# Kernel tuning notes

Hardware: AMD Instinct MI355X
Metric: run time of the kernel (lower is better)

The kernel has to match this reference:

```python
import jax, jax.numpy as jnp
import numpy as np

EPS = 1e-5

def layer_norm(x, gamma):
    mu = jnp.mean(x, axis=-1, keepdims=True)
    var = jnp.mean(jnp.square(x - mu), axis=-1, keepdims=True)
    return (x - mu) / jnp.sqrt(var + EPS) * gamma

def setup_inputs() -> dict:
    key = jax.random.key(0)
    ks = jax.random.split(key, 10)
    b, n, j = 2, 2048, 2048
    dim, ctx_dim, heads, dim_head, ff_mult = 1024, 1024, 16, 64, 4
    inner = heads * dim_head
    ff_inner = ff_mult * dim
    s = 0.02
    return {
        'x': jax.random.normal(ks[0], (b, n, dim), jnp.float32),
        'context': jax.random.normal(ks[1], (b, j, ctx_dim), jnp.float32),
        'mask': jax.random.randint(ks[2], (b, j), 0, 2, jnp.int32),
        'gamma': jnp.ones((dim,), jnp.float32),
        'ctx_gamma': jnp.ones((ctx_dim,), jnp.float32),
        'Wq': jax.random.normal(ks[3], (dim, inner), jnp.float32) * s,
        'Wkv': jax.random.normal(ks[4], (ctx_dim, 2 * dim_head), jnp.float32) * s,
        'Wout': jax.random.normal(ks[5], (inner, dim), jnp.float32) * s,
        'Wff1': jax.random.normal(ks[6], (dim, 2 * ff_inner), jnp.float32) * s,
        'Wff2': jax.random.normal(ks[7], (ff_inner, dim), jnp.float32) * s,
    }

def reference(x, context, mask, gamma, ctx_gamma, Wq, Wkv, Wout, Wff1, Wff2):
    heads, dim_head = 16, 64
    b, n, dim = x.shape
    scale = dim_head ** -0.5
    xn = layer_norm(x, gamma)                              # [b,n,dim]
    ctx = layer_norm(context, ctx_gamma)                   # [b,j,cd]
    q = (xn @ Wq).reshape(b, n, heads, dim_head).transpose(0, 2, 1, 3) * scale  # [b,h,n,d]
    kv = ctx @ Wkv                                         # [b,j,2d]
    k, v = kv[..., :dim_head], kv[..., dim_head:]          # [b,j,d] each (multi-query)
    sim = jnp.einsum('bhid,bjd->bhij', q, k)               # [b,h,n,j]
    sim = jnp.where((mask == 0)[:, None, None, :], -jnp.inf, sim)
    attn = jax.nn.softmax(sim, axis=-1)
    out = jnp.einsum('bhij,bjd->bhid', attn, v)            # [b,h,n,d]
    out = out.transpose(0, 2, 1, 3).reshape(b, n, heads * dim_head)
    out = out @ Wout                                       # [b,n,dim]
    # parallel SwiGLU FF on normalized x
    h = xn @ Wff1
    ff_inner = Wff2.shape[0]
    a, gate = h[..., :ff_inner], h[..., ff_inner:]
    out = out + (jax.nn.silu(gate) * a) @ Wff2
    return out
```

## Files before the change

kernel.cpp:

```cpp
#include <hip/hip_runtime.h>

typedef unsigned short u16;
typedef unsigned int   u32;
typedef __bf16  bf16x8 __attribute__((ext_vector_type(8)));
typedef __bf16  bf16x2 __attribute__((ext_vector_type(2)));
typedef float   f32x4  __attribute__((ext_vector_type(4)));

static __device__ __forceinline__ float b2f(u16 v) {
    return __builtin_bit_cast(float, (u32)(((u32)v) << 16));
}
static __device__ __forceinline__ u16 f2b(float f) {
    u32 u = __builtin_bit_cast(u32, f);
    return (u16)((u + 0x7FFFu + ((u >> 16) & 1u)) >> 16);
}
static __device__ __forceinline__ u32 pack2(float a, float b) {
    bf16x2 t; t[0] = (__bf16)a; t[1] = (__bf16)b;
    return __builtin_bit_cast(u32, t);
}

__global__ __launch_bounds__(256)
void ln_kernel(const float* __restrict__ x, const float* __restrict__ ctx,
               const float* __restrict__ gamma, const float* __restrict__ cgamma,
               u16* __restrict__ xn, u16* __restrict__ ctxn)
{
    const int row = blockIdx.x;
    const int tid = threadIdx.x;
    const float* src; const float* g; u16* dst;
    if (row < 4096) { src = x   + (long)row * 1024;          g = gamma;  dst = xn   + (long)row * 1024; }
    else            { src = ctx + (long)(row - 4096) * 1024; g = cgamma; dst = ctxn + (long)(row - 4096) * 1024; }
    float4 v = ((const float4*)src)[tid];
    float s = v.x + v.y + v.z + v.w;
    float q = v.x*v.x + v.y*v.y + v.z*v.z + v.w*v.w;
#pragma unroll
    for (int off = 32; off; off >>= 1) { s += __shfl_xor(s, off); q += __shfl_xor(q, off); }
    __shared__ float r1[4], r2[4];
    if ((tid & 63) == 0) { r1[tid >> 6] = s; r2[tid >> 6] = q; }
    __syncthreads();
    s = r1[0] + r1[1] + r1[2] + r1[3];
    q = r2[0] + r2[1] + r2[2] + r2[3];
    float mu   = s * (1.0f / 1024.0f);
    float var  = q * (1.0f / 1024.0f) - mu * mu;
    float rstd = rsqrtf(var + 1e-5f);
    float4 gv = ((const float4*)g)[tid];
    ushort4 o;
    o.x = f2b((v.x - mu) * rstd * gv.x);
    o.y = f2b((v.y - mu) * rstd * gv.y);
    o.z = f2b((v.z - mu) * rstd * gv.z);
    o.w = f2b((v.w - mu) * rstd * gv.w);
    ((ushort4*)dst)[tid] = o;
}

__global__ __launch_bounds__(256)
void wconv(const float* __restrict__ W, u16* __restrict__ Wt, int N, int K, float scale)
{
    __shared__ float tile[32][33];
    const int tid = threadIdx.x;
    const int n0 = blockIdx.x * 32;
    const int k0 = blockIdx.y * 32;
    const int r  = tid >> 3;
    const int c4 = (tid & 7) * 4;
    float4 v = *(const float4*)&W[(long)(k0 + r) * N + n0 + c4];
    tile[r][c4 + 0] = v.x; tile[r][c4 + 1] = v.y; tile[r][c4 + 2] = v.z; tile[r][c4 + 3] = v.w;
    __syncthreads();
    ushort4 o;
    o.x = f2b(tile[c4 + 0][r] * scale);
    o.y = f2b(tile[c4 + 1][r] * scale);
    o.z = f2b(tile[c4 + 2][r] * scale);
    o.w = f2b(tile[c4 + 3][r] * scale);
    *(ushort4*)&Wt[(long)(n0 + r) * K + k0 + c4] = o;
}

__global__ __launch_bounds__(256)
void wconv_ff1(const float* __restrict__ W, u16* __restrict__ Wt)
{
    __shared__ float tile[32][33];
    const int tid = threadIdx.x;
    const int a  = blockIdx.x;
    const int k0 = blockIdx.y * 32;
    const int r  = tid >> 3;
    const int c4 = (tid & 7) * 4;
    const int srccol = (c4 < 16) ? (a * 16 + c4) : (4096 + a * 16 + (c4 - 16));
    float4 v = *(const float4*)&W[(long)(k0 + r) * 8192 + srccol];
    tile[r][c4 + 0] = v.x; tile[r][c4 + 1] = v.y; tile[r][c4 + 2] = v.z; tile[r][c4 + 3] = v.w;
    __syncthreads();
    ushort4 o;
    o.x = f2b(tile[c4 + 0][r]);
    o.y = f2b(tile[c4 + 1][r]);
    o.z = f2b(tile[c4 + 2][r]);
    o.w = f2b(tile[c4 + 3][r]);
    *(ushort4*)&Wt[(long)(a * 32 + r) * 1024 + k0 + c4] = o;
}

__global__ __launch_bounds__(256)
void kext_build(const float* __restrict__ kvf, const int* __restrict__ mask,
                u16* __restrict__ kext, float* __restrict__ mbias)
{
    const int gid = blockIdx.x * 256 + threadIdx.x;
    const int b = gid >> 14;
    const int rem = gid & 16383;
    const int j = rem >> 3;
    const int c = rem & 7;
    const float* src = &kvf[((long)b * 2048 + j) * 128 + c * 8];
    u16 ov[8];
#pragma unroll
    for (int e = 0; e < 8; ++e) ov[e] = f2b(src[e]);
    uint4 w;
    w.x = (u32)ov[0] | ((u32)ov[1] << 16);
    w.y = (u32)ov[2] | ((u32)ov[3] << 16);
    w.z = (u32)ov[4] | ((u32)ov[5] << 16);
    w.w = (u32)ov[6] | ((u32)ov[7] << 16);
    *(uint4*)&kext[((long)b * 2048 + j) * 64 + c * 8] = w;
    if (c == 0) mbias[b * 2048 + j] = mask[b * 2048 + j] ? 0.0f : -1e30f;
}

__global__ __launch_bounds__(256)
void vtrans(const float* __restrict__ kvf, u16* __restrict__ vT)
{
    const int j = blockIdx.x * 256 + threadIdx.x;
    const int d = blockIdx.y;
    const int b = blockIdx.z;
    vT[(long)b * 64 * 2048 + (long)d * 2048 + j] =
        f2b(kvf[((long)b * 2048 + j) * 128 + 64 + d]);
}

#define BM 128
#define BN 128
#define BK 32

template<int EPI>
__global__ __launch_bounds__(256, 2)
void gemm_bt(const u16* __restrict__ A, const u16* __restrict__ Bt,
             void* __restrict__ Cv,
             int K, int lda, int ldb, int ldc,
             long aH, long bH, long cH)
{
    __shared__ __align__(16) u16 sm[2][2][BM * BK];
    const int tid  = threadIdx.x;
    const int wave = tid >> 6;
    const int lane = tid & 63;
    const int tn = blockIdx.x * BN;
    const int tm = blockIdx.y * BM;
    const int z  = blockIdx.z;
    A  += (long)z * aH;
    Bt += (long)z * bH;

    const int arow0 = (tid >> 2);
    const int arow1 = 64 + (tid >> 2);
    const int acs0  = (tid & 3) ^ ((arow0 >> 1) & 3);
    const int acs1  = (tid & 3) ^ ((arow1 >> 1) & 3);
    const int nt = K / BK;

#define STAGE(buf, k0)                                                                              \
    do {                                                                                            \
        __builtin_amdgcn_global_load_lds(                                                           \
            (const __attribute__((address_space(1))) void*)(A + (long)(tm + arow0) * lda + (k0) + acs0 * 8),   \
            (__attribute__((address_space(3))) void*)(&sm[buf][0][(wave * 64) * 8]), 16, 0, 0);     \
        __builtin_amdgcn_global_load_lds(                                                           \
            (const __attribute__((address_space(1))) void*)(A + (long)(tm + arow1) * lda + (k0) + acs1 * 8),   \
            (__attribute__((address_space(3))) void*)(&sm[buf][0][(256 + wave * 64) * 8]), 16, 0, 0); \
        __builtin_amdgcn_global_load_lds(                                                           \
            (const __attribute__((address_space(1))) void*)(Bt + (long)(tn + arow0) * ldb + (k0) + acs0 * 8),  \
            (__attribute__((address_space(3))) void*)(&sm[buf][1][(wave * 64) * 8]), 16, 0, 0);     \
        __builtin_amdgcn_global_load_lds(                                                           \
            (const __attribute__((address_space(1))) void*)(Bt + (long)(tn + arow1) * ldb + (k0) + acs1 * 8),  \
            (__attribute__((address_space(3))) void*)(&sm[buf][1][(256 + wave * 64) * 8]), 16, 0, 0); \
    } while (0)

    STAGE(0, 0);

    f32x4 acc[4][4] = {};
    const int wr   = (wave >> 1) * 64;
    const int wc   = (wave & 1) * 64;
    const int frow = lane & 15;
    const int fk   = lane >> 4;

    for (int t = 0; t < nt; ++t) {
        __syncthreads();
        if (t + 1 < nt) STAGE((t + 1) & 1, (t + 1) * BK);
        const int cur = t & 1;
        bf16x8 af[4], bf[4];
#pragma unroll
        for (int m = 0; m < 4; ++m) {
            int row = wr + m * 16 + frow;
            af[m] = *(const bf16x8*)&sm[cur][0][row * BK + ((fk ^ ((row >> 1) & 3)) * 8)];
        }
#pragma unroll
        for (int n = 0; n < 4; ++n) {
            int row = wc + n * 16 + frow;
            bf[n] = *(const bf16x8*)&sm[cur][1][row * BK + ((fk ^ ((row >> 1) & 3)) * 8)];
        }
#pragma unroll
        for (int m = 0; m < 4; ++m)
#pragma unroll
            for (int n = 0; n < 4; ++n)
                acc[m][n] = __builtin_amdgcn_mfma_f32_16x16x32_bf16(af[m], bf[n], acc[m][n], 0, 0, 0);
    }
#undef STAGE

    const long coff = (long)z * cH;
#pragma unroll
    for (int m = 0; m < 4; ++m) {
        const int row0 = tm + wr + m * 16 + fk * 4;
#pragma unroll
        for (int n = 0; n < 4; ++n) {
            const int col = tn + wc + n * 16 + frow;
#pragma unroll
            for (int r = 0; r < 4; ++r) {
                const long off = coff + (long)(row0 + r) * ldc + col;
                const float v = acc[m][n][r];
                if constexpr (EPI == 0)      ((u16*)Cv)[off] = f2b(v);
                else if constexpr (EPI == 1) ((float*)Cv)[off] = v;
                else if constexpr (EPI == 2) ((float*)Cv)[off] += v;
                else                         atomicAdd(&((float*)Cv)[off], v);
            }
        }
    }
}

template<int EPI>
__global__ __launch_bounds__(512, 2)
void gemm256(const u16* __restrict__ A, const u16* __restrict__ Bt,
             void* __restrict__ Cv, int K, int lda, int ldb, int ldc,
             long aH, long bH)
{
    __shared__ __align__(16) u16 As[2][256 * 64];
    __shared__ __align__(16) u16 Bs[2][256 * 64];
    const int tid  = threadIdx.x;
    const int wave = tid >> 6, lane = tid & 63;
    const int wm = wave >> 2, wn = wave & 3;
    const int frow = lane & 15, fk = lane >> 4;
    const int tn = blockIdx.x * 256;
    const int tm = blockIdx.y * 256;
    const int z  = blockIdx.z;
    A  += (long)z * aH;
    Bt += (long)z * bH;
    const int nt = K >> 6;

    const int lrow  = lane >> 3;
    const int csrc8 = ((lane & 7) ^ lrow) * 8;
    int rbA0[2], rbA1[2], rbB0[2], rbB1[2];
#pragma unroll
    for (int g = 0; g < 2; ++g) {
        const int c = g * 8 + wave;
        const int a0 = ((c >> 3) * 128) + ((c & 7) * 8);
        rbA0[g] = a0; rbA1[g] = a0 + 64;
        const int b0 = ((c >> 2) * 64) + ((c & 3) * 8);
        rbB0[g] = b0; rbB1[g] = b0 + 32;
    }

#define STG(LDS, buf, src, toff, ld, kt, rb)                                                        \
    __builtin_amdgcn_global_load_lds(                                                               \
        (const __attribute__((address_space(1))) void*)((src) + (long)((toff) + (rb) + lrow) * (ld) + ((kt) << 6) + csrc8), \
        (__attribute__((address_space(3))) void*)(&LDS[buf][(rb) * 64]), 16, 0, 0)

#define STAGE_A0(buf, kt) do { STG(As, buf, A,  tm, lda, kt, rbA0[0]); STG(As, buf, A,  tm, lda, kt, rbA0[1]); } while (0)
#define STAGE_A1(buf, kt) do { STG(As, buf, A,  tm, lda, kt, rbA1[0]); STG(As, buf, A,  tm, lda, kt, rbA1[1]); } while (0)
#define STAGE_B0(buf, kt) do { STG(Bs, buf, Bt, tn, ldb, kt, rbB0[0]); STG(Bs, buf, Bt, tn, ldb, kt, rbB0[1]); } while (0)
#define STAGE_B1(buf, kt) do { STG(Bs, buf, Bt, tn, ldb, kt, rbB1[0]); STG(Bs, buf, Bt, tn, ldb, kt, rbB1[1]); } while (0)

#define DSREAD_A(dst, half)                                                                         \
    do { _Pragma("unroll") for (int i = 0; i < 4; ++i) {                                            \
        const int row = wm * 128 + (half) * 64 + i * 16 + frow;                                     \
        _Pragma("unroll") for (int kk = 0; kk < 2; ++kk)                                            \
            dst[i][kk] = *(const bf16x8*)&As[cur][row * 64 + (((kk * 4 + fk) ^ (row & 7)) * 8)];    \
    } } while (0)
#define DSREAD_B(dst, half)                                                                         \
    do { _Pragma("unroll") for (int j = 0; j < 2; ++j) {                                            \
        const int row = wn * 64 + (half) * 32 + j * 16 + frow;                                      \
        _Pragma("unroll") for (int kk = 0; kk < 2; ++kk)                                            \
            dst[j][kk] = *(const bf16x8*)&Bs[cur][row * 64 + (((kk * 4 + fk) ^ (row & 7)) * 8)];    \
    } } while (0)
#define MFMA_Q(afr, bfr, mh, nh)                                                                    \
    do { __builtin_amdgcn_s_setprio(1);                                                             \
    _Pragma("unroll") for (int kk = 0; kk < 2; ++kk)                                                \
        _Pragma("unroll") for (int i = 0; i < 4; ++i)                                               \
            _Pragma("unroll") for (int j = 0; j < 2; ++j)                                           \
                acc[(mh) * 4 + i][(nh) * 2 + j] = __builtin_amdgcn_mfma_f32_16x16x32_bf16(          \
                    afr[i][kk], bfr[j][kk], acc[(mh) * 4 + i][(nh) * 2 + j], 0, 0, 0);              \
    __builtin_amdgcn_s_setprio(0); } while (0)
#define LGKM0 do { asm volatile("s_waitcnt lgkmcnt(0)" ::: "memory"); __builtin_amdgcn_sched_barrier(0); } while (0)
#define SB    __builtin_amdgcn_sched_barrier(0)
#define BAR   __builtin_amdgcn_s_barrier()

    STAGE_B0(0, 0); STAGE_A0(0, 0); STAGE_A1(0, 0); STAGE_B1(0, 0);
    if (nt > 1) {
        STAGE_B0(1, 1); STAGE_A0(1, 1);
        asm volatile("s_waitcnt vmcnt(4)" ::: "memory");
    } else {
        asm volatile("s_waitcnt vmcnt(0)" ::: "memory");
    }
    SB;
    BAR;

    f32x4 acc[8][4] = {};
    bf16x8 a0f[4][2], a1f[4][2], b0f[2][2], b1f[2][2];

    for (int t = 0; t < nt; ++t) {
        const int cur = t & 1, nxt = cur ^ 1;
        DSREAD_A(a0f, 0); DSREAD_B(b0f, 0);
        if (t + 1 < nt) STAGE_A1(nxt, t + 1);
        BAR; LGKM0;
        MFMA_Q(a0f, b0f, 0, 0);
        SB; BAR;
        DSREAD_B(b1f, 1);
        if (t + 1 < nt) STAGE_B1(nxt, t + 1);
        BAR; LGKM0;
        MFMA_Q(a0f, b1f, 0, 1);
        SB; BAR;
        DSREAD_A(a1f, 1);
        if (t + 2 < nt) STAGE_B0(cur, t + 2);
        BAR; LGKM0;
        MFMA_Q(a1f, b1f, 1, 1);
        SB; BAR;
        if (t + 2 < nt) STAGE_A0(cur, t + 2);
        BAR;
        MFMA_Q(a1f, b0f, 1, 0);
        SB;
        if (t + 1 < nt) {
            if (t + 2 < nt) asm volatile("s_waitcnt vmcnt(4)" ::: "memory");
            else            asm volatile("s_waitcnt vmcnt(0)" ::: "memory");
            SB;
            BAR;
        }
    }
#undef BAR
#undef SB
#undef LGKM0
#undef MFMA_Q
#undef DSREAD_A
#undef DSREAD_B
#undef STAGE_A0
#undef STAGE_A1
#undef STAGE_B0
#undef STAGE_B1
#undef STG

    if constexpr (EPI == 3) {
        u16* C = (u16*)Cv;
#pragma unroll
        for (int mf = 0; mf < 8; ++mf) {
            const int gr = tm + wm * 128 + mf * 16 + fk * 4;
#pragma unroll
            for (int np = 0; np < 4; np += 2) {
                const int scol = (tn >> 1) + (wn * 2 + (np >> 1)) * 16 + frow;
                const f32x4 av = acc[mf][np];
                const f32x4 gv = acc[mf][np + 1];
#pragma unroll
                for (int r = 0; r < 4; ++r) {
                    const float g = gv[r];
                    const float o = av[r] * g / (1.0f + __expf(-g));
                    C[(long)(gr + r) * ldc + scol] = f2b(o);
                }
            }
        }
    } else {
        float* C = (float*)Cv;
#pragma unroll
        for (int mf = 0; mf < 8; ++mf) {
            const int gr = tm + wm * 128 + mf * 16 + fk * 4;
#pragma unroll
            for (int nf = 0; nf < 4; ++nf) {
                const int col = tn + wn * 64 + nf * 16 + frow;
#pragma unroll
                for (int r = 0; r < 4; ++r)
                    atomicAdd(&C[(long)(gr + r) * ldc + col], acc[mf][nf][r]);
            }
        }
    }
}

__global__ __launch_bounds__(256, 4)
void flash_attn(const u16* __restrict__ qb, const u16* __restrict__ kext,
                const u16* __restrict__ vT, const float* __restrict__ mbias,
                u16* __restrict__ aout)
{
    __shared__ __align__(16) u16 Ksm[2][4096];
    __shared__ __align__(16) u16 Vsm[2][4096];
    __shared__ __align__(16) u16 Psm[4][1024];
    const int tid  = threadIdx.x;
    const int wave = tid >> 6, lane = tid & 63;
    const int frow = lane & 15, fk = lane >> 4;
    const int b = blockIdx.z, h = blockIdx.y;
    const int q0 = blockIdx.x * 64;

    const u16* kx = kext + (long)b * 2048 * 64;
    const u16* vb = vT   + (long)b * 64 * 2048;
    const float* mbb = mbias + b * 2048;

    const u16* qbase = qb + ((long)(b * 2048 + q0 + wave * 16 + frow)) * 1024 + h * 64;
    bf16x8 bq[2];
#pragma unroll
    for (int kk = 0; kk < 2; ++kk)
        bq[kk] = *(const bf16x8*)&qbase[kk * 32 + fk * 8];

#define FSTAGE(buf, j0s)                                                                             \
    do {                                                                                             \
        _Pragma("unroll")                                                                            \
        for (int i = 0; i < 2; ++i) {                                                                \
            const int slot = i * 256 + tid;                                                          \
            const int row  = slot >> 3;                                                              \
            const int csrc = (slot & 7) ^ (row & 7);                                                 \
            __builtin_amdgcn_global_load_lds(                                                        \
                (const __attribute__((address_space(1))) void*)(kx + (long)((j0s) + row) * 64 + csrc * 8), \
                (__attribute__((address_space(3))) void*)(&Ksm[buf][(i * 256 + wave * 64) * 8]), 16, 0, 0); \
            __builtin_amdgcn_global_load_lds(                                                        \
                (const __attribute__((address_space(1))) void*)(vb + (long)row * 2048 + (j0s) + csrc * 8),  \
                (__attribute__((address_space(3))) void*)(&Vsm[buf][(i * 256 + wave * 64) * 8]), 16, 0, 0); \
        }                                                                                            \
    } while (0)

    FSTAGE(0, 0);

    f32x4 oacc[4] = {};
    float mrun = -1e30f, lrun = 0.0f;
    u16* pw = &Psm[wave][0];

    for (int it = 0; it < 32; ++it) {
        const int j0 = it * 64;
        __syncthreads();
        float4 mb[4];
#pragma unroll
        for (int m = 0; m < 4; ++m)
            mb[m] = *(const float4*)&mbb[j0 + m * 16 + fk * 4];
        if (it + 1 < 32) FSTAGE((it + 1) & 1, (it + 1) * 64);
        const int cur = it & 1;

        f32x4 st[4] = {};
        __builtin_amdgcn_s_setprio(1);
#pragma unroll
        for (int kk = 0; kk < 2; ++kk) {
            bf16x8 ka[4];
#pragma unroll
            for (int m = 0; m < 4; ++m) {
                const int row = m * 16 + frow;
                ka[m] = *(const bf16x8*)&Ksm[cur][row * 64 + (((kk * 4 + fk) ^ (row & 7)) * 8)];
            }
#pragma unroll
            for (int m = 0; m < 4; ++m)
                st[m] = __builtin_amdgcn_mfma_f32_16x16x32_bf16(ka[m], bq[kk], st[m], 0, 0, 0);
        }
        __builtin_amdgcn_s_setprio(0);

        float sb[4][4];
#pragma unroll
        for (int m = 0; m < 4; ++m)
#pragma unroll
            for (int r = 0; r < 4; ++r) sb[m][r] = st[m][r] + (&mb[m].x)[r];
        float pm = fmaxf(
            fmaxf(fmaxf(sb[0][0], sb[0][1]), fmaxf(sb[0][2], sb[0][3])),
            fmaxf(fmaxf(sb[1][0], sb[1][1]), fmaxf(sb[1][2], sb[1][3])));
        pm = fmaxf(pm, fmaxf(
            fmaxf(fmaxf(sb[2][0], sb[2][1]), fmaxf(sb[2][2], sb[2][3])),
            fmaxf(fmaxf(sb[3][0], sb[3][1]), fmaxf(sb[3][2], sb[3][3]))));
        pm = fmaxf(pm, __shfl_xor(pm, 16));
        pm = fmaxf(pm, __shfl_xor(pm, 32));
        const float nm = fmaxf(mrun, pm);
        const float alpha = __expf(mrun - nm);
        mrun = nm;

        float rs = 0.0f;
#pragma unroll
        for (int m = 0; m < 4; ++m) {
            const float p0 = __expf(sb[m][0] - nm);
            const float p1 = __expf(sb[m][1] - nm);
            const float p2 = __expf(sb[m][2] - nm);
            const float p3 = __expf(sb[m][3] - nm);
            rs += (p0 + p1) + (p2 + p3);
            const int chunk = (m * 2 + (fk >> 1)) ^ (frow & 7);
            uint2 w; w.x = pack2(p0, p1); w.y = pack2(p2, p3);
            *(uint2*)&pw[frow * 64 + chunk * 8 + (fk & 1) * 4] = w;
        }
        rs += __shfl_xor(rs, 16);
        rs += __shfl_xor(rs, 32);
        lrun = lrun * alpha + rs;
#pragma unroll
        for (int mo = 0; mo < 4; ++mo)
#pragma unroll
            for (int r = 0; r < 4; ++r) oacc[mo][r] *= alpha;

        __builtin_amdgcn_s_setprio(1);
#pragma unroll
        for (int kkv = 0; kkv < 2; ++kkv) {
            bf16x8 va[4];
#pragma unroll
            for (int mo = 0; mo < 4; ++mo) {
                const int row = mo * 16 + frow;
                va[mo] = *(const bf16x8*)&Vsm[cur][row * 64 + (((kkv * 4 + fk) ^ (row & 7)) * 8)];
            }
            const bf16x8 pb = *(const bf16x8*)&pw[frow * 64 + (((kkv * 4 + fk) ^ (frow & 7)) * 8)];
#pragma unroll
            for (int mo = 0; mo < 4; ++mo)
                oacc[mo] = __builtin_amdgcn_mfma_f32_16x16x32_bf16(va[mo], pb, oacc[mo], 0, 0, 0);
        }
        __builtin_amdgcn_s_setprio(0);
    }
#undef FSTAGE

    const float inv = 1.0f / lrun;
    const long row = (long)b * 2048 + q0 + wave * 16 + frow;
#pragma unroll
    for (int mo = 0; mo < 4; ++mo) {
        uint2 w;
        w.x = pack2(oacc[mo][0] * inv, oacc[mo][1] * inv);
        w.y = pack2(oacc[mo][2] * inv, oacc[mo][3] * inv);
        *(uint2*)&aout[row * 1024 + h * 64 + mo * 16 + fk * 4] = w;
    }
}

extern "C" void kernel_launch(void* const* d_in, const int* in_sizes, int n_in,
                              void* d_out, int out_size, void* d_ws, size_t ws_size,
                              hipStream_t stream)
{
    const float* x      = (const float*)d_in[0];
    const float* ctx    = (const float*)d_in[1];
    const int*   mask   = (const int*)d_in[2];
    const float* gamma  = (const float*)d_in[3];
    const float* cgamma = (const float*)d_in[4];
    const float* Wq     = (const float*)d_in[5];
    const float* Wkv    = (const float*)d_in[6];
    const float* Wout   = (const float*)d_in[7];
    const float* Wff1   = (const float*)d_in[8];
    const float* Wff2   = (const float*)d_in[9];
    float* out = (float*)d_out;

    char* w = (char*)d_ws;
    auto carveB = [&](long bytes) { char* p = w; w += ((bytes + 255) / 256) * 256; return p; };
    u16*   xn     = (u16*)  carveB(4096L * 1024 * 2);
    u16*   ctxn   = (u16*)  carveB(4096L * 1024 * 2);
    u16*   WqT    = (u16*)  carveB(1024L * 1024 * 2);
    u16*   WkvT   = (u16*)  carveB(128L * 1024 * 2);
    u16*   WoutT  = (u16*)  carveB(1024L * 1024 * 2);
    u16*   Wff1Tp = (u16*)  carveB(8192L * 1024 * 2);
    u16*   Wff2T  = (u16*)  carveB(1024L * 4096 * 2);
    u16*   q      = (u16*)  carveB(4096L * 1024 * 2);
    float* kvf    = (float*)carveB(2L * 2048 * 128 * 4);
    u16*   kext   = (u16*)  carveB(2L * 2048 * 64 * 2);
    float* mbias  = (float*)carveB(2L * 2048 * 4);
    u16*   vT     = (u16*)  carveB(2L * 64 * 2048 * 2);
    u16*   aout   = (u16*)  carveB(4096L * 1024 * 2);
    u16*   gbuf   = (u16*)  carveB(4096L * 4096 * 2);

    dim3 B(256);

    ln_kernel<<<dim3(8192), B, 0, stream>>>(x, ctx, gamma, cgamma, xn, ctxn);
    wconv<<<dim3(32, 32),  B, 0, stream>>>(Wq,   WqT,   1024, 1024, 0.125f);
    wconv<<<dim3(4, 32),   B, 0, stream>>>(Wkv,  WkvT,  128,  1024, 1.0f);
    wconv<<<dim3(32, 32),  B, 0, stream>>>(Wout, WoutT, 1024, 1024, 1.0f);
    wconv_ff1<<<dim3(256, 32), B, 0, stream>>>(Wff1, Wff1Tp);
    wconv<<<dim3(32, 128), B, 0, stream>>>(Wff2, Wff2T, 1024, 4096, 1.0f);

    gemm_bt<0><<<dim3(8, 32, 1), B, 0, stream>>>(xn, WqT, q, 1024, 1024, 1024, 1024, 0, 0, 0);
    hipMemsetAsync(kvf, 0, 2L * 2048 * 128 * 4, stream);
    gemm_bt<4><<<dim3(1, 32, 4), B, 0, stream>>>(ctxn, WkvT, kvf, 256, 1024, 1024, 128, 256, 256, 0);
    kext_build<<<dim3(128), B, 0, stream>>>(kvf, mask, kext, mbias);
    vtrans<<<dim3(8, 64, 2), B, 0, stream>>>(kvf, vT);

    flash_attn<<<dim3(32, 16, 2), B, 0, stream>>>(q, kext, vT, mbias, aout);

    gemm_bt<1><<<dim3(8, 32, 1), B, 0, stream>>>(aout, WoutT, out, 1024, 1024, 1024, 1024, 0, 0, 0);
    gemm256<3><<<dim3(32, 16, 1), dim3(512), 0, stream>>>(xn, Wff1Tp, gbuf, 1024, 1024, 1024, 4096, 0, 0);
    gemm256<4><<<dim3(4, 16, 4), dim3(512), 0, stream>>>(gbuf, Wff2T, out, 1024, 4096, 4096, 1024, 1024, 1024);
}
```

Before: 423.2 us.

## Fuse output projection and FF2 into one K=5120 GEMM via concatenated buffers

Attention output and the SwiGLU activations are written side by side into one [4096,5120] buffer, and Wout and Wff2 are transposed into one concatenated [1024,5120] weight. A single gemm_bt with K=5120 then produces the final output directly. This replaces the separate Wout GEMM and the split-K atomicAdd FF2 GEMM, removing the atomics and an extra pass over the output. The cost is that the combined GEMM now runs on the smaller 128-tile gemm_bt kernel over a long K, which may be less efficient than the 256-tile kernel and gets less parallelism, with only 256 blocks.

```diff
diff --git a/kernel.cpp b/kernel.cpp
--- a/kernel.cpp
+++ b/kernel.cpp
@@ -51,7 +51,8 @@
 }
 
 __global__ __launch_bounds__(256)
-void wconv(const float* __restrict__ W, u16* __restrict__ Wt, int N, int K, float scale)
+void wconv(const float* __restrict__ W, u16* __restrict__ Wt, int N, int K,
+           int ldout, int koff, float scale)
 {
     __shared__ float tile[32][33];
     const int tid = threadIdx.x;
@@ -67,7 +68,7 @@
     o.y = f2b(tile[c4 + 1][r] * scale);
     o.z = f2b(tile[c4 + 2][r] * scale);
     o.w = f2b(tile[c4 + 3][r] * scale);
-    *(ushort4*)&Wt[(long)(n0 + r) * K + k0 + c4] = o;
+    *(ushort4*)&Wt[(long)(n0 + r) * ldout + koff + k0 + c4] = o;
 }
 
 __global__ __launch_bounds__(256)
@@ -217,11 +218,9 @@
     }
 }
 
-template<int EPI>
 __global__ __launch_bounds__(512, 2)
-void gemm256(const u16* __restrict__ A, const u16* __restrict__ Bt,
-             void* __restrict__ Cv, int K, int lda, int ldb, int ldc,
-             long aH, long bH)
+void gemm256_ff1(const u16* __restrict__ A, const u16* __restrict__ Bt,
+                 u16* __restrict__ C, int K, int lda, int ldb, int ldc)
 {
     __shared__ __align__(16) u16 As[2][256 * 64];
     __shared__ __align__(16) u16 Bs[2][256 * 64];
@@ -231,9 +230,6 @@
     const int frow = lane & 15, fk = lane >> 4;
     const int tn = blockIdx.x * 256;
     const int tm = blockIdx.y * 256;
-    const int z  = blockIdx.z;
-    A  += (long)z * aH;
-    Bt += (long)z * bH;
     const int nt = K >> 6;
 
     const int lrow  = lane >> 3;
@@ -335,35 +331,19 @@
 #undef STAGE_B1
 #undef STG
 
-    if constexpr (EPI == 3) {
-        u16* C = (u16*)Cv;
-#pragma unroll
-        for (int mf = 0; mf < 8; ++mf) {
-            const int gr = tm + wm * 128 + mf * 16 + fk * 4;
-#pragma unroll
-            for (int np = 0; np < 4; np += 2) {
-                const int scol = (tn >> 1) + (wn * 2 + (np >> 1)) * 16 + frow;
-                const f32x4 av = acc[mf][np];
-                const f32x4 gv = acc[mf][np + 1];
-#pragma unroll
-                for (int r = 0; r < 4; ++r) {
-                    const float g = gv[r];
-                    const float o = av[r] * g / (1.0f + __expf(-g));
-                    C[(long)(gr + r) * ldc + scol] = f2b(o);
-                }
-            }
-        }
-    } else {
-        float* C = (float*)Cv;
-#pragma unroll
-        for (int mf = 0; mf < 8; ++mf) {
-            const int gr = tm + wm * 128 + mf * 16 + fk * 4;
-#pragma unroll
-            for (int nf = 0; nf < 4; ++nf) {
-                const int col = tn + wn * 64 + nf * 16 + frow;
-#pragma unroll
-                for (int r = 0; r < 4; ++r)
-                    atomicAdd(&C[(long)(gr + r) * ldc + col], acc[mf][nf][r]);
+#pragma unroll
+    for (int mf = 0; mf < 8; ++mf) {
+        const int gr = tm + wm * 128 + mf * 16 + fk * 4;
+#pragma unroll
+        for (int np = 0; np < 4; np += 2) {
+            const int scol = (tn >> 1) + (wn * 2 + (np >> 1)) * 16 + frow;
+            const f32x4 av = acc[mf][np];
+            const f32x4 gv = acc[mf][np + 1];
+#pragma unroll
+            for (int r = 0; r < 4; ++r) {
+                const float g = gv[r];
+                const float o = av[r] * g / (1.0f + __expf(-g));
+                C[(long)(gr + r) * ldc + scol] = f2b(o);
             }
         }
     }
@@ -372,7 +352,7 @@
 __global__ __launch_bounds__(256, 4)
 void flash_attn(const u16* __restrict__ qb, const u16* __restrict__ kext,
                 const u16* __restrict__ vT, const float* __restrict__ mbias,
-                u16* __restrict__ aout)
+                u16* __restrict__ aout, int ldo)
 {
     __shared__ __align__(16) u16 Ksm[2][4096];
     __shared__ __align__(16) u16 Vsm[2][4096];
@@ -503,7 +483,7 @@
         uint2 w;
         w.x = pack2(oacc[mo][0] * inv, oacc[mo][1] * inv);
         w.y = pack2(oacc[mo][2] * inv, oacc[mo][3] * inv);
-        *(uint2*)&aout[row * 1024 + h * 64 + mo * 16 + fk * 4] = w;
+        *(uint2*)&aout[row * ldo + h * 64 + mo * 16 + fk * 4] = w;
     }
 }
 
@@ -529,25 +509,23 @@
     u16*   ctxn   = (u16*)  carveB(4096L * 1024 * 2);
     u16*   WqT    = (u16*)  carveB(1024L * 1024 * 2);
     u16*   WkvT   = (u16*)  carveB(128L * 1024 * 2);
-    u16*   WoutT  = (u16*)  carveB(1024L * 1024 * 2);
+    u16*   bigW   = (u16*)  carveB(1024L * 5120 * 2);
     u16*   Wff1Tp = (u16*)  carveB(8192L * 1024 * 2);
-    u16*   Wff2T  = (u16*)  carveB(1024L * 4096 * 2);
     u16*   q      = (u16*)  carveB(4096L * 1024 * 2);
     float* kvf    = (float*)carveB(2L * 2048 * 128 * 4);
     u16*   kext   = (u16*)  carveB(2L * 2048 * 64 * 2);
     float* mbias  = (float*)carveB(2L * 2048 * 4);
     u16*   vT     = (u16*)  carveB(2L * 64 * 2048 * 2);
-    u16*   aout   = (u16*)  carveB(4096L * 1024 * 2);
-    u16*   gbuf   = (u16*)  carveB(4096L * 4096 * 2);
+    u16*   comb   = (u16*)  carveB(4096L * 5120 * 2);
 
     dim3 B(256);
 
     ln_kernel<<<dim3(8192), B, 0, stream>>>(x, ctx, gamma, cgamma, xn, ctxn);
-    wconv<<<dim3(32, 32),  B, 0, stream>>>(Wq,   WqT,   1024, 1024, 0.125f);
-    wconv<<<dim3(4, 32),   B, 0, stream>>>(Wkv,  WkvT,  128,  1024, 1.0f);
-    wconv<<<dim3(32, 32),  B, 0, stream>>>(Wout, WoutT, 1024, 1024, 1.0f);
+    wconv<<<dim3(32, 32),  B, 0, stream>>>(Wq,   WqT,  1024, 1024, 1024, 0,    0.125f);
+    wconv<<<dim3(4, 32),   B, 0, stream>>>(Wkv,  WkvT, 128,  1024, 1024, 0,    1.0f);
+    wconv<<<dim3(32, 32),  B, 0, stream>>>(Wout, bigW, 1024, 1024, 5120, 0,    1.0f);
+    wconv<<<dim3(32, 128), B, 0, stream>>>(Wff2, bigW, 1024, 4096, 5120, 1024, 1.0f);
     wconv_ff1<<<dim3(256, 32), B, 0, stream>>>(Wff1, Wff1Tp);
-    wconv<<<dim3(32, 128), B, 0, stream>>>(Wff2, Wff2T, 1024, 4096, 1.0f);
 
     gemm_bt<0><<<dim3(8, 32, 1), B, 0, stream>>>(xn, WqT, q, 1024, 1024, 1024, 1024, 0, 0, 0);
     hipMemsetAsync(kvf, 0, 2L * 2048 * 128 * 4, stream);
@@ -555,9 +533,9 @@
     kext_build<<<dim3(128), B, 0, stream>>>(kvf, mask, kext, mbias);
     vtrans<<<dim3(8, 64, 2), B, 0, stream>>>(kvf, vT);
 
-    flash_attn<<<dim3(32, 16, 2), B, 0, stream>>>(q, kext, vT, mbias, aout);
-
-    gemm_bt<1><<<dim3(8, 32, 1), B, 0, stream>>>(aout, WoutT, out, 1024, 1024, 1024, 1024, 0, 0, 0);
-    gemm256<3><<<dim3(32, 16, 1), dim3(512), 0, stream>>>(xn, Wff1Tp, gbuf, 1024, 1024, 1024, 4096, 0, 0);
-    gemm256<4><<<dim3(4, 16, 4), dim3(512), 0, stream>>>(gbuf, Wff2T, out, 1024, 4096, 4096, 1024, 1024, 1024);
-}
+    flash_attn<<<dim3(32, 16, 2), B, 0, stream>>>(q, kext, vT, mbias, comb, 5120);
+
+    gemm256_ff1<<<dim3(32, 16), dim3(512), 0, stream>>>(xn, Wff1Tp, comb + 1024, 1024, 1024, 1024, 5120);
+
+    gemm_bt<1><<<dim3(8, 32, 1), B, 0, stream>>>(comb, bigW, out, 5120, 5120, 5120, 1024, 0, 0, 0);
+}
```

Result: faster. 410.8 us (-2.9%).
